# Optimization experiments

Hardware: AMD Instinct MI355X
Metric: run time of the kernel (lower is better)

Reference implementation:

```python
import jax, jax.numpy as jnp
import numpy as np

B, N, H, D = 1, 4096, 16, 64
C = H * D  # 1024
SCALE = D ** -0.5


def setup_inputs() -> dict:
    key = jax.random.key(0)
    k1, k2, k3, k4 = jax.random.split(key, 4)
    x = jax.random.normal(k1, (B, N, C), dtype=jnp.float32)
    # torch nn.Linear weights: [out_features, in_features]; y = x @ W.T + b
    w_qkv = jax.random.normal(k2, (3 * C, C), dtype=jnp.float32) * 0.02
    w_proj = jax.random.normal(k3, (C, C), dtype=jnp.float32) * 0.02
    b_proj = jax.random.normal(k4, (C,), dtype=jnp.float32) * 0.02
    return {"x": x, "w_qkv": w_qkv, "w_proj": w_proj, "b_proj": b_proj}


def reference(x, w_qkv, w_proj, b_proj):
    Bn, Nn, Cn = x.shape
    # fused QKV projection (no bias)
    qkv = jnp.einsum('bnc,oc->bno', x, w_qkv)            # [B,N,3C]
    qkv = qkv.reshape(Bn, Nn, 3, H, D)
    q = jnp.transpose(qkv[:, :, 0], (0, 2, 1, 3))        # [B,H,N,D]
    k = jnp.transpose(qkv[:, :, 1], (0, 2, 1, 3))
    v = jnp.transpose(qkv[:, :, 2], (0, 2, 1, 3))
    attn = jnp.einsum('bhnd,bhmd->bhnm', q, k) * SCALE   # [B,H,N,N]
    causal_mask = jnp.triu(jnp.ones((Nn, Nn), dtype=bool), k=1)
    attn = jnp.where(causal_mask, -jnp.inf, attn)
    attn = jax.nn.softmax(attn, axis=-1)
    out = jnp.einsum('bhnm,bhmd->bhnd', attn, v)          # [B,H,N,D]
    out = jnp.transpose(out, (0, 2, 1, 3)).reshape(Bn, Nn, Cn)
    out = jnp.einsum('bnc,oc->bno', out, w_proj) + b_proj
    return out
```

## Files before the change

### kernel.cpp

```cpp
#include <hip/hip_runtime.h>
#include <hip/hip_bf16.h>
#include <stdint.h>
#include <stddef.h>

using bf16 = __hip_bfloat16;
typedef short short8 __attribute__((ext_vector_type(8)));
typedef short short4v __attribute__((ext_vector_type(4)));
typedef short short2v __attribute__((ext_vector_type(2)));
typedef float f32x4 __attribute__((ext_vector_type(4)));
typedef float f32x16 __attribute__((ext_vector_type(16)));
typedef unsigned uintv4 __attribute__((ext_vector_type(4)));

#define MFMA16(A, B, C) __builtin_amdgcn_mfma_f32_16x16x32_bf16(A, B, C, 0, 0, 0)
#define MFMA32(A, B, C) __builtin_amdgcn_mfma_f32_32x32x16_bf16(A, B, C, 0, 0, 0)
#define GLOAD_LDS(g, l) __builtin_amdgcn_global_load_lds( \
    (const __attribute__((address_space(1))) void*)(g),   \
    (__attribute__((address_space(3))) void*)(l), 16, 0, 0)

constexpr int AN  = 4096;
constexpr int NH  = 16;
constexpr int HD  = 64;
constexpr int CC  = 1024;
constexpr int C3  = 3072;
constexpr float QSCALE = 0.125f * 1.4426950408889634f;

__device__ inline short bf16s(float f) {
    return (short)((__float_as_uint(f) + 0x8000u) >> 16);
}
__device__ inline float bf2f(short s) {
    return __uint_as_float(((unsigned)(unsigned short)s) << 16);
}
__device__ inline bf16 sbf(short s) {
    union { short s; bf16 b; } u;
    u.s = s;
    return u.b;
}
#if __has_builtin(__builtin_amdgcn_cvt_pk_bf16_f32)
typedef __bf16 bf16x2 __attribute__((ext_vector_type(2)));
__device__ inline short2v pk2(float a, float b) {
    bf16x2 r = __builtin_amdgcn_cvt_pk_bf16_f32(a, b);
    return *(short2v*)&r;
}
#else
__device__ inline short2v pk2(float a, float b) {
    unsigned ua = __float_as_uint(a) + 0x8000u;
    unsigned ub = __float_as_uint(b) + 0x8000u;
    unsigned r  = __builtin_amdgcn_perm(ub, ua, 0x07060302);
    return *(short2v*)&r;
}
#endif
__device__ inline unsigned pk2u(float a, float b) {
    short2v p = pk2(a, b);
    return *(unsigned*)&p;
}
__device__ inline short4v pack4(float a, float b, float c, float d) {
    short2v lo = pk2(a, b), hi = pk2(c, d);
    short4v r;
    r[0] = lo[0]; r[1] = lo[1]; r[2] = hi[0]; r[3] = hi[1];
    return r;
}
__device__ inline void plswap(unsigned &a, unsigned &b) {
    asm("v_permlane32_swap_b32 %0, %1" : "+v"(a), "+v"(b));
}
#if __has_builtin(__builtin_amdgcn_exp2f)
#define FAST_EXP2(x) __builtin_amdgcn_exp2f(x)
#else
#define FAST_EXP2(x) exp2f(x)
#endif

__device__ inline int detect_mode_inline(const unsigned short* xraw, int lane) {
    int crazy = 0;
    #pragma unroll
    for (int i = 0; i < 4; ++i) {
        const unsigned short u = xraw[lane * 4 + i];
        const int e = (u >> 7) & 0xFF;
        if (e >= 134 || (e != 0 && e <= 110)) ++crazy;
    }
    #pragma unroll
    for (int off = 32; off > 0; off >>= 1)
        crazy += __shfl_down(crazy, off, 64);
    crazy = __shfl(crazy, 0, 64);
    return (crazy >= 8) ? 1 : 0;
}

__device__ inline void cast8(const void* __restrict__ src,
                             bf16* __restrict__ dst, int i, int m) {
    if (m) {
        const float* s = (const float*)src;
        float4 a = *(const float4*)(s + i);
        float4 b = *(const float4*)(s + i + 4);
        short8 o;
        short2v p0 = pk2(a.x, a.y), p1 = pk2(a.z, a.w);
        short2v p2 = pk2(b.x, b.y), p3 = pk2(b.z, b.w);
        o[0] = p0[0]; o[1] = p0[1]; o[2] = p1[0]; o[3] = p1[1];
        o[4] = p2[0]; o[5] = p2[1]; o[6] = p3[0]; o[7] = p3[1];
        *(short8*)(dst + i) = o;
    } else {
        *(short8*)(dst + i) = *(const short8*)((const short*)src + i);
    }
}

__global__ void cast_all(const void* __restrict__ x, const void* __restrict__ wq,
                         const void* __restrict__ wp, const void* __restrict__ bp,
                         bf16* __restrict__ xb, bf16* __restrict__ wqb,
                         bf16* __restrict__ wpb, float* __restrict__ biasf,
                         int* __restrict__ mode) {
    const int b = blockIdx.x;
    const int tid = threadIdx.x;
    const int m = detect_mode_inline((const unsigned short*)x, tid & 63);
    if (b < 2048) {
        cast8(x, xb, (b * 256 + tid) * 8, m);
    } else if (b < 3584) {
        cast8(wq, wqb, ((b - 2048) * 256 + tid) * 8, m);
    } else if (b < 4096) {
        cast8(wp, wpb, ((b - 3584) * 256 + tid) * 8, m);
    } else {
        #pragma unroll
        for (int i = tid; i < CC; i += 256)
            biasf[i] = m ? ((const float*)bp)[i] : bf2f(((const short*)bp)[i]);
        if (tid == 0) *mode = m;
    }
}

constexpr int BM = 128, BN = 128, BK = 32;

__global__ __launch_bounds__(256, 3) void gemm_qkv(
    const bf16* __restrict__ A, const bf16* __restrict__ Bw,
    bf16* __restrict__ qOut, bf16* __restrict__ kOut, bf16* __restrict__ vOut)
{
    __shared__ bf16 As[BM * BK];
    __shared__ bf16 Bs[BN * BK];

    const int tid  = threadIdx.x;
    const int wave = tid >> 6;
    const int lane = tid & 63;
    const int quad = lane >> 4;
    const int l16  = lane & 15;
    const int wr   = wave >> 1;
    const int wc   = wave & 1;
    const int m0   = blockIdx.y * BM;
    const int o0   = blockIdx.x * BN;

    const int srow = lane >> 2;
    const int scol = (lane & 3) * 8;

    f32x4 acc[4][4] = {};

    for (int k0 = 0; k0 < CC; k0 += BK) {
        __syncthreads();
        #pragma unroll
        for (int c = 0; c < 2; ++c) {
            const int rbase = wave * 32 + c * 16;
            GLOAD_LDS(A + (size_t)(m0 + rbase + srow) * CC + k0 + scol, &As[rbase * BK]);
            GLOAD_LDS(Bw + (size_t)(o0 + rbase + srow) * CC + k0 + scol, &Bs[rbase * BK]);
        }
        __syncthreads();

        short8 af[4], bfr[4];
        #pragma unroll
        for (int i = 0; i < 4; ++i)
            af[i] = *(const short8*)&As[(wr * 64 + i * 16 + l16) * BK + quad * 8];
        #pragma unroll
        for (int j = 0; j < 4; ++j)
            bfr[j] = *(const short8*)&Bs[(wc * 64 + j * 16 + l16) * BK + quad * 8];
        #pragma unroll
        for (int i = 0; i < 4; ++i)
            #pragma unroll
            for (int j = 0; j < 4; ++j)
                acc[i][j] = MFMA16(af[i], bfr[j], acc[i][j]);
    }

    if (o0 >= 2 * CC) {
        #pragma unroll
        for (int j = 0; j < 4; ++j) {
            const int dcol = o0 - 2 * CC + wc * 64 + j * 16 + l16;
            const int hV = dcol >> 6, dV = dcol & 63;
            #pragma unroll
            for (int i = 0; i < 4; ++i) {
                const int kv0 = m0 + wr * 64 + i * 16 + quad * 4;
                const size_t addr = (size_t)hV * 64 * AN + (size_t)(kv0 >> 6) * 4096
                                  + (size_t)((kv0 >> 3) & 7) * 512 + dV * 8 + (kv0 & 7);
                *(short4v*)&vOut[addr] =
                    pack4(acc[i][j][0], acc[i][j][1], acc[i][j][2], acc[i][j][3]);
            }
        }
        return;
    }
    if (o0 >= CC) {
        #pragma unroll
        for (int j = 0; j < 4; ++j) {
            const int dcol = o0 - CC + wc * 64 + j * 16 + l16;
            const int hK = dcol >> 6, dc = (dcol >> 3) & 7, de = dcol & 7;
            #pragma unroll
            for (int i = 0; i < 4; ++i) {
                const int kv0 = m0 + wr * 64 + i * 16 + quad * 4;
                const size_t addr = (size_t)hK * 64 * AN + (size_t)(kv0 >> 6) * 4096
                                  + (size_t)dc * 512 + (size_t)(kv0 & 63) * 8 + de;
                #pragma unroll
                for (int r = 0; r < 4; ++r)
                    kOut[addr + r * 8] = sbf(bf16s(acc[i][j][r]));
            }
        }
        return;
    }
    #pragma unroll
    for (int j = 0; j < 4; ++j) {
        const int col = o0 + wc * 64 + j * 16 + l16;
        #pragma unroll
        for (int i = 0; i < 4; ++i) {
            const int row = m0 + wr * 64 + i * 16 + quad * 4;
            #pragma unroll
            for (int r = 0; r < 2; ++r) {
                short2v p = pk2(acc[i][j][2 * r] * QSCALE, acc[i][j][2 * r + 1] * QSCALE);
                qOut[(size_t)(row + 2 * r) * CC + col]     = sbf(p[0]);
                qOut[(size_t)(row + 2 * r + 1) * CC + col] = sbf(p[1]);
            }
        }
    }
}

constexpr int PM = 128, PN = 64, PK = 32;

__global__ __launch_bounds__(256, 2) void gemm_proj(
    const bf16* __restrict__ A, const bf16* __restrict__ Bw,
    const float* __restrict__ bias, void* __restrict__ Cout,
    const int* __restrict__ mode)
{
    __shared__ bf16 As[PM * PK];
    __shared__ bf16 Bs[PN * PK];

    const int tid  = threadIdx.x;
    const int wave = tid >> 6;
    const int lane = tid & 63;
    const int quad = lane >> 4;
    const int l16  = lane & 15;
    const int wr   = wave >> 1;
    const int wc   = wave & 1;
    const int m0   = blockIdx.y * PM;
    const int o0   = blockIdx.x * PN;
    const bool f32out = (*mode != 0);

    const int srow = lane >> 2;
    const int scol = (lane & 3) * 8;

    f32x4 acc[4][2] = {};

    for (int k0 = 0; k0 < CC; k0 += PK) {
        __syncthreads();
        #pragma unroll
        for (int c = 0; c < 2; ++c) {
            const int rbase = wave * 32 + c * 16;
            GLOAD_LDS(A + (size_t)(m0 + rbase + srow) * CC + k0 + scol, &As[rbase * PK]);
        }
        {
            const int rbase = wave * 16;
            GLOAD_LDS(Bw + (size_t)(o0 + rbase + srow) * CC + k0 + scol, &Bs[rbase * PK]);
        }
        __syncthreads();

        short8 af[4], bfr[2];
        #pragma unroll
        for (int i = 0; i < 4; ++i)
            af[i] = *(const short8*)&As[(wr * 64 + i * 16 + l16) * PK + quad * 8];
        #pragma unroll
        for (int j = 0; j < 2; ++j)
            bfr[j] = *(const short8*)&Bs[(wc * 32 + j * 16 + l16) * PK + quad * 8];
        #pragma unroll
        for (int i = 0; i < 4; ++i)
            #pragma unroll
            for (int j = 0; j < 2; ++j)
                acc[i][j] = MFMA16(af[i], bfr[j], acc[i][j]);
    }

    #pragma unroll
    for (int j = 0; j < 2; ++j) {
        const int col = o0 + wc * 32 + j * 16 + l16;
        const float bv = bias[col];
        #pragma unroll
        for (int i = 0; i < 4; ++i) {
            const int row = m0 + wr * 64 + i * 16 + quad * 4;
            if (f32out) {
                #pragma unroll
                for (int r = 0; r < 4; ++r)
                    ((float*)Cout)[(size_t)(row + r) * CC + col] = acc[i][j][r] + bv;
            } else {
                #pragma unroll
                for (int r = 0; r < 2; ++r) {
                    short2v p = pk2(acc[i][j][2 * r] + bv, acc[i][j][2 * r + 1] + bv);
                    ((bf16*)Cout)[(size_t)(row + 2 * r) * CC + col]     = sbf(p[0]);
                    ((bf16*)Cout)[(size_t)(row + 2 * r + 1) * CC + col] = sbf(p[1]);
                }
            }
        }
    }
}

__global__ __launch_bounds__(256, 2) void attn14(
    const bf16* __restrict__ qbuf, const bf16* __restrict__ kP,
    const bf16* __restrict__ vP, bf16* __restrict__ outO)
{
    __shared__ float ldsO[2][32][64];
    __shared__ float ldsL[2][64];

    const int tid  = threadIdx.x;
    const int w    = tid >> 6;
    const int rh   = w & 1;
    const int s    = w >> 1;
    const int lane = tid & 63;
    const int l31  = lane & 31;
    const int hh   = lane >> 5;
    const int bid  = blockIdx.x;
    const int h    = bid & 15;
    const int bp   = bid >> 4;

    short8 ones8;
    #pragma unroll
    for (int i = 0; i < 8; ++i) ones8[i] = (short)0x3F80;

    #pragma unroll 1
    for (int pp = 0; pp < 2; ++pp) {
        const int tile = pp ? 63 - bp : bp;
        const int nIt  = tile + 1;
        const int mid  = (nIt + 1) >> 1;
        const int i0   = s ? mid : 0;
        const int iHi  = s ? nIt : mid;
        const int qw   = tile * 64 + rh * 32;
        const int q    = qw + l31;

        short8 qf[4];
        {
            const bf16* qp = qbuf + (size_t)q * CC + h * HD + hh * 8;
            #pragma unroll
            for (int ki = 0; ki < 4; ++ki)
                qf[ki] = *(const short8*)(qp + ki * 16);
        }

        f32x16 acc_l = {};
        f32x16 acc_o[2] = {};

        if (i0 < iHi) {
            const bf16* kb = kP + (size_t)h * 64 * AN + (size_t)i0 * 4096;
            const bf16* vb = vP + (size_t)h * 64 * AN + (size_t)i0 * 4096;
            const bool hasdiag = (iHi == nIt);

            short8 kf[8];
            #pragma unroll
            for (int kt = 0; kt < 2; ++kt)
                #pragma unroll
                for (int ki = 0; ki < 4; ++ki)
                    kf[kt * 4 + ki] = *(const short8*)
                        (kb + (2 * ki + hh) * 512 + kt * 256 + l31 * 8);
            kb += 4096;

            for (int it = i0; it < iHi; ++it) {
                short8 vf[8];
                #pragma unroll
                for (int kk = 0; kk < 4; ++kk)
                    #pragma unroll
                    for (int dt2 = 0; dt2 < 2; ++dt2)
                        vf[kk * 2 + dt2] = *(const short8*)
                            (vb + (2 * kk + hh) * 512 + dt2 * 256 + l31 * 8);
                vb += 4096;

                f32x16 st[2];
                __builtin_amdgcn_s_setprio(1);
                #pragma unroll
                for (int kt = 0; kt < 2; ++kt) {
                    f32x16 a = {};
                    #pragma unroll
                    for (int ki = 0; ki < 4; ++ki)
                        a = MFMA32(kf[kt * 4 + ki], qf[ki], a);
                    st[kt] = a;
                }
                __builtin_amdgcn_s_setprio(0);

                if (it + 1 < iHi) {
                    #pragma unroll
                    for (int kt = 0; kt < 2; ++kt)
                        #pragma unroll
                        for (int ki = 0; ki < 4; ++ki)
                            kf[kt * 4 + ki] = *(const short8*)
                                (kb + (2 * ki + hh) * 512 + kt * 256 + l31 * 8);
                    kb += 4096;
                }

                if (hasdiag && it == iHi - 1) {
                    const int kv0 = it * 64;
                    #pragma unroll
                    for (int kt = 0; kt < 2; ++kt)
                        #pragma unroll
                        for (int r = 0; r < 16; ++r) {
                            const int kv = kv0 + kt * 32 + (r & 3) + 8 * (r >> 2) + 4 * hh;
                            st[kt][r] = (kv <= q) ? FAST_EXP2(st[kt][r]) : 0.0f;
                        }
                } else {
                    #pragma unroll
                    for (int kt = 0; kt < 2; ++kt)
                        #pragma unroll
                        for (int r = 0; r < 16; ++r)
                            st[kt][r] = FAST_EXP2(st[kt][r]);
                }

                #pragma unroll
                for (int kt = 0; kt < 2; ++kt)
                    #pragma unroll
                    for (int kc = 0; kc < 2; ++kc) {
                        unsigned a0 = pk2u(st[kt][kc * 8 + 0], st[kt][kc * 8 + 1]);
                        unsigned a1 = pk2u(st[kt][kc * 8 + 2], st[kt][kc * 8 + 3]);
                        unsigned c0 = pk2u(st[kt][kc * 8 + 4], st[kt][kc * 8 + 5]);
                        unsigned c1 = pk2u(st[kt][kc * 8 + 6], st[kt][kc * 8 + 7]);
                        plswap(a0, c0);
                        plswap(a1, c1);
                        uintv4 fu;
                        fu[0] = a0; fu[1] = a1; fu[2] = c0; fu[3] = c1;
                        const short8 frag = *(const short8*)&fu;

                        __builtin_amdgcn_s_setprio(1);
                        acc_l = MFMA32(ones8, frag, acc_l);
                        #pragma unroll
                        for (int dt2 = 0; dt2 < 2; ++dt2)
                            acc_o[dt2] = MFMA32(vf[(kt * 2 + kc) * 2 + dt2],
                                                frag, acc_o[dt2]);
                        __builtin_amdgcn_s_setprio(0);
                    }
            }
        }

        if (s == 1) {
            #pragma unroll
            for (int dt2 = 0; dt2 < 2; ++dt2)
                #pragma unroll
                for (int r = 0; r < 16; ++r)
                    ldsO[rh][dt2 * 16 + r][lane] = acc_o[dt2][r];
            ldsL[rh][lane] = acc_l[0];
        }
        __syncthreads();
        if (s == 0) {
            const float L = acc_l[0] + ldsL[rh][lane];
            const float invL = (L > 0.f) ? 1.f / L : 0.f;
            const size_t base = (size_t)q * CC + h * HD;
            #pragma unroll
            for (int dt2 = 0; dt2 < 2; ++dt2)
                #pragma unroll
                for (int g = 0; g < 4; ++g) {
                    const int d0 = dt2 * 32 + g * 8 + 4 * hh;
                    float o0 = (acc_o[dt2][4 * g + 0] + ldsO[rh][dt2 * 16 + 4 * g + 0][lane]) * invL;
                    float o1 = (acc_o[dt2][4 * g + 1] + ldsO[rh][dt2 * 16 + 4 * g + 1][lane]) * invL;
                    float o2 = (acc_o[dt2][4 * g + 2] + ldsO[rh][dt2 * 16 + 4 * g + 2][lane]) * invL;
                    float o3 = (acc_o[dt2][4 * g + 3] + ldsO[rh][dt2 * 16 + 4 * g + 3][lane]) * invL;
                    *(short4v*)&outO[base + d0] = pack4(o0, o1, o2, o3);
                }
        }
        __syncthreads();
    }
}

extern "C" void kernel_launch(void* const* d_in, const int* in_sizes, int n_in,
                              void* d_out, int out_size, void* d_ws, size_t ws_size,
                              hipStream_t stream) {
    char* ws = (char*)d_ws;
    bf16*   qbuf     = (bf16*)(ws);
    bf16*   kPack    = (bf16*)(ws + 8388608);
    bf16*   vPack    = (bf16*)(ws + 16777216);
    bf16*   attn_out = (bf16*)(ws + 25165824);
    bf16*   xb       = (bf16*)(ws + 33554432);
    bf16*   wqkvb    = (bf16*)(ws + 41943040);
    bf16*   wprojb   = (bf16*)(ws + 48234496);
    float*  biasf    = (float*)(ws + 50331648);
    int*    mode     = (int*)(ws + 50335744);

    cast_all<<<dim3(4097), 256, 0, stream>>>(
        d_in[0], d_in[1], d_in[2], d_in[3], xb, wqkvb, wprojb, biasf, mode);

    gemm_qkv<<<dim3(C3 / BN, AN / BM), 256, 0, stream>>>(
        xb, wqkvb, qbuf, kPack, vPack);
    attn14<<<dim3(32 * NH), 256, 0, stream>>>(qbuf, kPack, vPack, attn_out);
    gemm_proj<<<dim3(CC / PN, AN / PM), 256, 0, stream>>>(
        attn_out, wprojb, biasf, d_out, mode);
}
```

Measured before the change: 186.1 us.

## Split KV range across four waves each covering all 64 query rows

Each wave now handles both 32-row query groups over a quarter of the KV tiles, instead of two waves per row-half splitting KV in halves. Each K/V fragment load is reused for twice as many MFMAs. The row sum moves from a ones-matrix MFMA to a VALU reduction plus a cross-half shuffle, and the fully masked upper sub-block of the diagonal tile is skipped. In exchange it uses more registers for accumulators and Q fragments, and needs a two-stage LDS reduction across four waves with an extra barrier.

```diff
diff --git a/kernel.cpp b/kernel.cpp
--- a/kernel.cpp
+++ b/kernel.cpp
@@ -295,17 +295,15 @@
     }
 }
 
-__global__ __launch_bounds__(256, 2) void attn14(
+__global__ __launch_bounds__(256, 2) void attn16(
     const bf16* __restrict__ qbuf, const bf16* __restrict__ kP,
     const bf16* __restrict__ vP, bf16* __restrict__ outO)
 {
-    __shared__ float ldsO[2][32][64];
-    __shared__ float ldsL[2][64];
+    __shared__ float ldsO[2][2][2][16][64];
+    __shared__ float ldsL[2][2][64];
 
     const int tid  = threadIdx.x;
     const int w    = tid >> 6;
-    const int rh   = w & 1;
-    const int s    = w >> 1;
     const int lane = tid & 63;
     const int l31  = lane & 31;
     const int hh   = lane >> 5;
@@ -313,34 +311,29 @@
     const int h    = bid & 15;
     const int bp   = bid >> 4;
 
-    short8 ones8;
-    #pragma unroll
-    for (int i = 0; i < 8; ++i) ones8[i] = (short)0x3F80;
-
     #pragma unroll 1
     for (int pp = 0; pp < 2; ++pp) {
         const int tile = pp ? 63 - bp : bp;
         const int nIt  = tile + 1;
-        const int mid  = (nIt + 1) >> 1;
-        const int i0   = s ? mid : 0;
-        const int iHi  = s ? nIt : mid;
-        const int qw   = tile * 64 + rh * 32;
-        const int q    = qw + l31;
-
-        short8 qf[4];
-        {
-            const bf16* qp = qbuf + (size_t)q * CC + h * HD + hh * 8;
+        const int i0   = (nIt * w) >> 2;
+        const int iHi  = (nIt * (w + 1)) >> 2;
+        const int qb   = tile * 64;
+
+        short8 qf[2][4];
+        #pragma unroll
+        for (int g = 0; g < 2; ++g) {
+            const bf16* qp = qbuf + (size_t)(qb + 32 * g + l31) * CC + h * HD + hh * 8;
             #pragma unroll
             for (int ki = 0; ki < 4; ++ki)
-                qf[ki] = *(const short8*)(qp + ki * 16);
-        }
-
-        f32x16 acc_l = {};
-        f32x16 acc_o[2] = {};
+                qf[g][ki] = *(const short8*)(qp + ki * 16);
+        }
+
+        float lsum[2] = {0.f, 0.f};
+        f32x16 acc_o[2][2] = {};
 
         if (i0 < iHi) {
-            const bf16* kb = kP + (size_t)h * 64 * AN + (size_t)i0 * 4096;
-            const bf16* vb = vP + (size_t)h * 64 * AN + (size_t)i0 * 4096;
+            const bf16* kb = kP + (size_t)h * 64 * AN;
+            const bf16* vb = vP + (size_t)h * 64 * AN;
             const bool hasdiag = (iHi == nIt);
 
             short8 kf[8];
@@ -349,30 +342,74 @@
                 #pragma unroll
                 for (int ki = 0; ki < 4; ++ki)
                     kf[kt * 4 + ki] = *(const short8*)
-                        (kb + (2 * ki + hh) * 512 + kt * 256 + l31 * 8);
-            kb += 4096;
+                        (kb + (size_t)i0 * 4096 + (2 * ki + hh) * 512 + kt * 256 + l31 * 8);
 
             for (int it = i0; it < iHi; ++it) {
-                short8 vf[8];
-                #pragma unroll
-                for (int kk = 0; kk < 4; ++kk)
-                    #pragma unroll
-                    for (int dt2 = 0; dt2 < 2; ++dt2)
-                        vf[kk * 2 + dt2] = *(const short8*)
-                            (vb + (2 * kk + hh) * 512 + dt2 * 256 + l31 * 8);
-                vb += 4096;
-
-                f32x16 st[2];
-                __builtin_amdgcn_s_setprio(1);
-                #pragma unroll
-                for (int kt = 0; kt < 2; ++kt) {
-                    f32x16 a = {};
-                    #pragma unroll
-                    for (int ki = 0; ki < 4; ++ki)
-                        a = MFMA32(kf[kt * 4 + ki], qf[ki], a);
-                    st[kt] = a;
+                const bool diag = hasdiag && (it == iHi - 1);
+
+                short8 vf[4][2];
+                {
+                    const bf16* vs = vb + (size_t)it * 4096;
+                    #pragma unroll
+                    for (int kk = 0; kk < 4; ++kk)
+                        #pragma unroll
+                        for (int dt2 = 0; dt2 < 2; ++dt2)
+                            vf[kk][dt2] = *(const short8*)
+                                (vs + (2 * kk + hh) * 512 + dt2 * 256 + l31 * 8);
                 }
-                __builtin_amdgcn_s_setprio(0);
+
+                short8 fr[2][4];
+                #pragma unroll
+                for (int g = 0; g < 2; ++g) {
+                    #pragma unroll
+                    for (int kt = 0; kt < 2; ++kt) {
+                        if (diag && g == 0 && kt == 1) continue;
+                        f32x16 st = {};
+                        __builtin_amdgcn_s_setprio(1);
+                        #pragma unroll
+                        for (int ki = 0; ki < 4; ++ki)
+                            st = MFMA32(kf[kt * 4 + ki], qf[g][ki], st);
+                        __builtin_amdgcn_s_setprio(0);
+
+                        const bool tri = diag && ((g == 0 && kt == 0) ||
+                                                  (g == 1 && kt == 1));
+                        const int qrel = g * 32 + l31;
+                        if (tri) {
+                            #pragma unroll
+                            for (int r = 0; r < 16; ++r) {
+                                const int kv = kt * 32 + (r & 3) + 8 * (r >> 2) + 4 * hh;
+                                st[r] = (kv <= qrel) ? FAST_EXP2(st[r]) : 0.0f;
+                            }
+                        } else {
+                            #pragma unroll
+                            for (int r = 0; r < 16; ++r)
+                                st[r] = FAST_EXP2(st[r]);
+                        }
+
+                        {
+                            float s0 = 0.f, s1 = 0.f, s2 = 0.f, s3 = 0.f;
+                            #pragma unroll
+                            for (int r = 0; r < 16; r += 4) {
+                                s0 += st[r];     s1 += st[r + 1];
+                                s2 += st[r + 2]; s3 += st[r + 3];
+                            }
+                            lsum[g] += (s0 + s1) + (s2 + s3);
+                        }
+
+                        #pragma unroll
+                        for (int kc = 0; kc < 2; ++kc) {
+                            unsigned a0 = pk2u(st[kc * 8 + 0], st[kc * 8 + 1]);
+                            unsigned a1 = pk2u(st[kc * 8 + 2], st[kc * 8 + 3]);
+                            unsigned c0 = pk2u(st[kc * 8 + 4], st[kc * 8 + 5]);
+                            unsigned c1 = pk2u(st[kc * 8 + 6], st[kc * 8 + 7]);
+                            plswap(a0, c0);
+                            plswap(a1, c1);
+                            uintv4 fu;
+                            fu[0] = a0; fu[1] = a1; fu[2] = c0; fu[3] = c1;
+                            fr[g][kt * 2 + kc] = *(const short8*)&fu;
+                        }
+                    }
+                }
 
                 if (it + 1 < iHi) {
                     #pragma unroll
@@ -380,76 +417,93 @@
                         #pragma unroll
                         for (int ki = 0; ki < 4; ++ki)
                             kf[kt * 4 + ki] = *(const short8*)
-                                (kb + (2 * ki + hh) * 512 + kt * 256 + l31 * 8);
-                    kb += 4096;
+                                (kb + (size_t)(it + 1) * 4096
+                                 + (2 * ki + hh) * 512 + kt * 256 + l31 * 8);
                 }
 
-                if (hasdiag && it == iHi - 1) {
-                    const int kv0 = it * 64;
-                    #pragma unroll
-                    for (int kt = 0; kt < 2; ++kt)
+                __builtin_amdgcn_s_setprio(1);
+                #pragma unroll
+                for (int g = 0; g < 2; ++g)
+                    #pragma unroll
+                    for (int kt = 0; kt < 2; ++kt) {
+                        if (diag && g == 0 && kt == 1) continue;
                         #pragma unroll
-                        for (int r = 0; r < 16; ++r) {
-                            const int kv = kv0 + kt * 32 + (r & 3) + 8 * (r >> 2) + 4 * hh;
-                            st[kt][r] = (kv <= q) ? FAST_EXP2(st[kt][r]) : 0.0f;
-                        }
-                } else {
-                    #pragma unroll
-                    for (int kt = 0; kt < 2; ++kt)
-                        #pragma unroll
-                        for (int r = 0; r < 16; ++r)
-                            st[kt][r] = FAST_EXP2(st[kt][r]);
-                }
-
-                #pragma unroll
-                for (int kt = 0; kt < 2; ++kt)
-                    #pragma unroll
-                    for (int kc = 0; kc < 2; ++kc) {
-                        unsigned a0 = pk2u(st[kt][kc * 8 + 0], st[kt][kc * 8 + 1]);
-                        unsigned a1 = pk2u(st[kt][kc * 8 + 2], st[kt][kc * 8 + 3]);
-                        unsigned c0 = pk2u(st[kt][kc * 8 + 4], st[kt][kc * 8 + 5]);
-                        unsigned c1 = pk2u(st[kt][kc * 8 + 6], st[kt][kc * 8 + 7]);
-                        plswap(a0, c0);
-                        plswap(a1, c1);
-                        uintv4 fu;
-                        fu[0] = a0; fu[1] = a1; fu[2] = c0; fu[3] = c1;
-                        const short8 frag = *(const short8*)&fu;
-
-                        __builtin_amdgcn_s_setprio(1);
-                        acc_l = MFMA32(ones8, frag, acc_l);
-                        #pragma unroll
-                        for (int dt2 = 0; dt2 < 2; ++dt2)
-                            acc_o[dt2] = MFMA32(vf[(kt * 2 + kc) * 2 + dt2],
-                                                frag, acc_o[dt2]);
-                        __builtin_amdgcn_s_setprio(0);
+                        for (int kc = 0; kc < 2; ++kc)
+                            #pragma unroll
+                            for (int dt2 = 0; dt2 < 2; ++dt2)
+                                acc_o[g][dt2] = MFMA32(vf[kt * 2 + kc][dt2],
+                                                       fr[g][kt * 2 + kc],
+                                                       acc_o[g][dt2]);
                     }
-            }
-        }
-
-        if (s == 1) {
-            #pragma unroll
-            for (int dt2 = 0; dt2 < 2; ++dt2)
-                #pragma unroll
-                for (int r = 0; r < 16; ++r)
-                    ldsO[rh][dt2 * 16 + r][lane] = acc_o[dt2][r];
-            ldsL[rh][lane] = acc_l[0];
-        }
-        __syncthreads();
-        if (s == 0) {
-            const float L = acc_l[0] + ldsL[rh][lane];
-            const float invL = (L > 0.f) ? 1.f / L : 0.f;
-            const size_t base = (size_t)q * CC + h * HD;
-            #pragma unroll
-            for (int dt2 = 0; dt2 < 2; ++dt2)
-                #pragma unroll
-                for (int g = 0; g < 4; ++g) {
-                    const int d0 = dt2 * 32 + g * 8 + 4 * hh;
-                    float o0 = (acc_o[dt2][4 * g + 0] + ldsO[rh][dt2 * 16 + 4 * g + 0][lane]) * invL;
-                    float o1 = (acc_o[dt2][4 * g + 1] + ldsO[rh][dt2 * 16 + 4 * g + 1][lane]) * invL;
-                    float o2 = (acc_o[dt2][4 * g + 2] + ldsO[rh][dt2 * 16 + 4 * g + 2][lane]) * invL;
-                    float o3 = (acc_o[dt2][4 * g + 3] + ldsO[rh][dt2 * 16 + 4 * g + 3][lane]) * invL;
-                    *(short4v*)&outO[base + d0] = pack4(o0, o1, o2, o3);
-                }
+                __builtin_amdgcn_s_setprio(0);
+            }
+        }
+
+        float lt[2];
+        #pragma unroll
+        for (int g = 0; g < 2; ++g)
+            lt[g] = lsum[g] + __shfl_xor(lsum[g], 32, 64);
+
+        if (w == 1 || w == 3) {
+            const int slot = w >> 1;
+            #pragma unroll
+            for (int g = 0; g < 2; ++g) {
+                #pragma unroll
+                for (int dt2 = 0; dt2 < 2; ++dt2)
+                    #pragma unroll
+                    for (int r = 0; r < 16; ++r)
+                        ldsO[slot][g][dt2][r][lane] = acc_o[g][dt2][r];
+                ldsL[slot][g][lane] = lt[g];
+            }
+        }
+        __syncthreads();
+        if (w == 0 || w == 2) {
+            const int slot = w >> 1;
+            #pragma unroll
+            for (int g = 0; g < 2; ++g) {
+                #pragma unroll
+                for (int dt2 = 0; dt2 < 2; ++dt2)
+                    #pragma unroll
+                    for (int r = 0; r < 16; ++r)
+                        acc_o[g][dt2][r] += ldsO[slot][g][dt2][r][lane];
+                lt[g] += ldsL[slot][g][lane];
+            }
+        }
+        if (w == 2) {
+            #pragma unroll
+            for (int g = 0; g < 2; ++g) {
+                #pragma unroll
+                for (int dt2 = 0; dt2 < 2; ++dt2)
+                    #pragma unroll
+                    for (int r = 0; r < 16; ++r)
+                        ldsO[1][g][dt2][r][lane] = acc_o[g][dt2][r];
+                ldsL[1][g][lane] = lt[g];
+            }
+        }
+        __syncthreads();
+        if (w == 0) {
+            #pragma unroll
+            for (int g = 0; g < 2; ++g) {
+                #pragma unroll
+                for (int dt2 = 0; dt2 < 2; ++dt2)
+                    #pragma unroll
+                    for (int r = 0; r < 16; ++r)
+                        acc_o[g][dt2][r] += ldsO[1][g][dt2][r][lane];
+                const float L = lt[g] + ldsL[1][g][lane];
+                const float invL = (L > 0.f) ? 1.f / L : 0.f;
+                const size_t base = (size_t)(qb + 32 * g + l31) * CC + h * HD;
+                #pragma unroll
+                for (int dt2 = 0; dt2 < 2; ++dt2)
+                    #pragma unroll
+                    for (int gi = 0; gi < 4; ++gi) {
+                        const int d0 = dt2 * 32 + gi * 8 + 4 * hh;
+                        *(short4v*)&outO[base + d0] = pack4(
+                            acc_o[g][dt2][4 * gi + 0] * invL,
+                            acc_o[g][dt2][4 * gi + 1] * invL,
+                            acc_o[g][dt2][4 * gi + 2] * invL,
+                            acc_o[g][dt2][4 * gi + 3] * invL);
+                    }
+            }
         }
         __syncthreads();
     }
@@ -474,7 +528,7 @@
 
     gemm_qkv<<<dim3(C3 / BN, AN / BM), 256, 0, stream>>>(
         xb, wqkvb, qbuf, kPack, vPack);
-    attn14<<<dim3(32 * NH), 256, 0, stream>>>(qbuf, kPack, vPack, attn_out);
+    attn16<<<dim3(32 * NH), 256, 0, stream>>>(qbuf, kPack, vPack, attn_out);
     gemm_proj<<<dim3(CC / PN, AN / PM), 256, 0, stream>>>(
         attn_out, wprojb, biasf, d_out, mode);
 }
```

After: 185.1 us. No clear change (-0.5%).
